# Kernel tuning notes

Hardware: AMD Instinct MI355X
Metric: run time of the kernel (lower is better)

The kernel has to match this reference:

```python
import jax, jax.numpy as jnp
import numpy as np

N_NODES = 100000
N_EDGES = 1600000
IN_CH = 128
HID = 128
OUT_CH = 2
NUM_GRAPHS = 512


def _mlp_params(key, d_in, d_out):
    k1, k2 = jax.random.split(key)
    s1 = 1.0 / np.sqrt(d_in)
    s2 = 1.0 / np.sqrt(d_out)
    return (jax.random.uniform(k1, (d_in, d_out), jnp.float32, -s1, s1),
            jnp.zeros((d_out,), jnp.float32),
            jax.random.uniform(k2, (d_out, d_out), jnp.float32, -s2, s2),
            jnp.zeros((d_out,), jnp.float32))


def setup_inputs() -> dict:
    key = jax.random.key(0)
    ks = jax.random.split(key, 8)
    x = jax.random.normal(ks[0], (N_NODES, IN_CH), jnp.float32)
    edge_index = jax.random.randint(ks[1], (2, N_EDGES), 0, N_NODES, jnp.int64)
    batch = jnp.sort(jax.random.randint(ks[2], (N_NODES,), 0, NUM_GRAPHS, jnp.int64))
    w1_0, b1_0, w2_0, b2_0 = _mlp_params(ks[3], IN_CH, HID)
    w1_1, b1_1, w2_1, b2_1 = _mlp_params(ks[4], HID, HID)
    w1_2, b1_2, w2_2, b2_2 = _mlp_params(ks[5], HID, HID)
    s = 1.0 / np.sqrt(HID)
    w_lin = jax.random.uniform(ks[6], (HID, OUT_CH), jnp.float32, -s, s)
    b_lin = jnp.zeros((OUT_CH,), jnp.float32)
    return {"x": x, "edge_index": edge_index, "batch": batch,
            "w1_0": w1_0, "b1_0": b1_0, "w2_0": w2_0, "b2_0": b2_0,
            "w1_1": w1_1, "b1_1": b1_1, "w2_1": w2_1, "b2_1": b2_1,
            "w1_2": w1_2, "b1_2": b1_2, "w2_2": w2_2, "b2_2": b2_2,
            "w_lin": w_lin, "b_lin": b_lin}


def _gin_conv(x, src, dst, w1, b1, w2, b2):
    # GINConv with eps=0: MLP(x + sum_{j in N(i)} x_j)
    agg = jax.ops.segment_sum(x[src], dst, num_segments=N_NODES)  # [N, d]
    h = x + agg
    h = jax.nn.relu(h @ w1 + b1)
    return h @ w2 + b2


def reference(x, edge_index, batch,
              w1_0, b1_0, w2_0, b2_0,
              w1_1, b1_1, w2_1, b2_1,
              w1_2, b1_2, w2_2, b2_2,
              w_lin, b_lin):
    src, dst = edge_index[0], edge_index[1]
    h = _gin_conv(x, src, dst, w1_0, b1_0, w2_0, b2_0)
    h = jax.nn.relu(h)
    h = jax.nn.relu(_gin_conv(h, src, dst, w1_1, b1_1, w2_1, b2_1))
    h = jax.nn.relu(h)  # forward applies relu twice after GIN1
    h = _gin_conv(h, src, dst, w1_2, b1_2, w2_2, b2_2)
    # global mean pool per graph
    sums = jax.ops.segment_sum(h, batch, num_segments=NUM_GRAPHS)  # [G, d]
    counts = jax.ops.segment_sum(jnp.ones((N_NODES,), h.dtype), batch,
                                 num_segments=NUM_GRAPHS)
    pooled = sums / jnp.maximum(counts, 1.0)[:, None]
    # dropout is identity in eval mode
    return pooled @ w_lin + b_lin  # [G, OUT_CH]
```

## Files before the change

### kernel.cpp

```cpp
#include <hip/hip_runtime.h>
#include <hip/hip_bf16.h>

#define N_NODES   100000
#define N_EDGES   1600000
#define IN_CH     128
#define HID       128
#define OUT_CH    2
#define NUM_GRAPHS 512

#define BKT_SHIFT 9
#define NB2 ((N_NODES + 511) >> BKT_SHIFT)
#define PB  200
#define CHUNK (N_EDGES / PB)

#define NCAST (N_NODES * IN_CH / 4 / 256)

typedef __attribute__((ext_vector_type(8))) short bf16x8;
typedef __attribute__((ext_vector_type(4))) float f32x4;
typedef unsigned int uint32;
typedef unsigned long long uint64;

static __device__ __forceinline__ float b2f(uint32 b) {
    return __uint_as_float(b << 16);
}
static __device__ __forceinline__ unsigned short f2b(float f) {
    uint32 u = __float_as_uint(f);
    u += 0x7fffu + ((u >> 16) & 1u);
    return (unsigned short)(u >> 16);
}
static __device__ __forceinline__ void acc8(float* a, int4 v) {
    uint32 x;
    x = (uint32)v.x; a[0] += __uint_as_float(x << 16); a[1] += __uint_as_float(x & 0xffff0000u);
    x = (uint32)v.y; a[2] += __uint_as_float(x << 16); a[3] += __uint_as_float(x & 0xffff0000u);
    x = (uint32)v.z; a[4] += __uint_as_float(x << 16); a[5] += __uint_as_float(x & 0xffff0000u);
    x = (uint32)v.w; a[6] += __uint_as_float(x << 16); a[7] += __uint_as_float(x & 0xffff0000u);
}

__global__ void k_front(const float* __restrict__ x, unsigned short* __restrict__ h,
                        const float* w0, const float* w1, const float* w2,
                        const float* w3, const float* w4, const float* w5,
                        unsigned short* __restrict__ wt,
                        const int* __restrict__ dst, int* __restrict__ histG) {
    __shared__ int hist[NB2];
    int bid = blockIdx.x, t = threadIdx.x;
    if (bid < NCAST) {
        int base = (bid * 256 + t) * 4;
        float4 v = *(const float4*)(x + base);
        ushort4 o;
        o.x = f2b(v.x); o.y = f2b(v.y); o.z = f2b(v.z); o.w = f2b(v.w);
        *(ushort4*)(h + base) = o;
    } else if (bid < NCAST + 6) {
        const float* ws[6] = {w0, w1, w2, w3, w4, w5};
        int wi = bid - NCAST;
        const float* w = ws[wi];
        unsigned short* o = wt + wi * 16384;
        for (int i = t; i < 16384; i += 256) {
            int k = i >> 7, n = i & 127;
            o[n * 128 + k] = f2b(w[i]);
        }
    } else {
        int blk = bid - NCAST - 6;
        for (int i = t; i < NB2; i += 256) hist[i] = 0;
        __syncthreads();
        int base = blk * CHUNK;
        for (int i = t; i < CHUNK; i += 256)
            atomicAdd(&hist[dst[base + i] >> BKT_SHIFT], 1);
        __syncthreads();
        for (int i = t; i < NB2; i += 256) histG[i * PB + blk] = hist[i];
    }
}

__global__ void k_scan1(const int* __restrict__ in, int* __restrict__ out,
                        int* __restrict__ bsum, int n) {
    __shared__ int sm[256];
    int b = blockIdx.x, t = threadIdx.x;
    int base = b * 1024 + t * 4;
    int v0 = 0, v1 = 0, v2 = 0, v3 = 0;
    if (base + 3 < n) {
        int4 q = *(const int4*)(in + base);
        v0 = q.x; v1 = q.y; v2 = q.z; v3 = q.w;
    } else {
        if (base + 0 < n) v0 = in[base + 0];
        if (base + 1 < n) v1 = in[base + 1];
        if (base + 2 < n) v2 = in[base + 2];
        if (base + 3 < n) v3 = in[base + 3];
    }
    int s = v0 + v1 + v2 + v3;
    sm[t] = s;
    __syncthreads();
    for (int off = 1; off < 256; off <<= 1) {
        int u = (t >= off) ? sm[t - off] : 0;
        __syncthreads();
        sm[t] += u;
        __syncthreads();
    }
    int p = (t == 0) ? 0 : sm[t - 1];
    int o0 = p, o1 = p + v0, o2 = o1 + v1, o3 = o2 + v2;
    if (base + 3 < n) {
        *(int4*)(out + base) = make_int4(o0, o1, o2, o3);
    } else {
        if (base + 0 < n) out[base + 0] = o0;
        if (base + 1 < n) out[base + 1] = o1;
        if (base + 2 < n) out[base + 2] = o2;
        if (base + 3 < n) out[base + 3] = o3;
    }
    if (t == 255) bsum[b] = s + ((t == 0) ? 0 : sm[t - 1]);
}

__global__ void k_scan3b(int* __restrict__ out, const int* __restrict__ bsum, int n) {
    __shared__ int add_s;
    int b = blockIdx.x, t = threadIdx.x;
    if (t == 0) {
        int s = 0;
        for (int i = 0; i < b; ++i) s += bsum[i];
        add_s = s;
    }
    __syncthreads();
    int add = add_s;
    int base = b * 1024 + t * 4;
    if (base + 3 < n) {
        int4 q = *(const int4*)(out + base);
        q.x += add; q.y += add; q.z += add; q.w += add;
        *(int4*)(out + base) = q;
    } else {
        for (int j = 0; j < 4; ++j)
            if (base + j < n) out[base + j] += add;
    }
}

__global__ void k_p3g(const int* __restrict__ ei, const int* __restrict__ baseG,
                      uint64* __restrict__ ebuf,
                      const int* __restrict__ batch, int* __restrict__ goff) {
    __shared__ int cur[NB2];
    int t = threadIdx.x, blk = blockIdx.x;
    if (blk >= PB) {
        int g = (blk - PB) * 512 + t;
        if (g <= NUM_GRAPHS) {
            int lo = 0, hi = N_NODES;
            while (lo < hi) {
                int mid = (lo + hi) >> 1;
                if (batch[mid] < g) lo = mid + 1; else hi = mid;
            }
            goff[g] = lo;
        }
        return;
    }
    for (int i = t; i < NB2; i += 512) cur[i] = baseG[i * PB + blk];
    __syncthreads();
    int base = blk * CHUNK;
    for (int i = t; i < CHUNK; i += 512) {
        int e = base + i;
        int src = ei[e];
        int dst = ei[N_EDGES + e];
        int pos = atomicAdd(&cur[dst >> BKT_SHIFT], 1);
        ebuf[pos] = ((uint64)(uint32)dst << 32) | (uint32)src;
    }
}

__global__ void k_p4(const uint64* __restrict__ ebuf, const int* __restrict__ baseG,
                     int* __restrict__ off, int* __restrict__ csr) {
    __shared__ int ldeg[512];
    __shared__ int lscan[512];
    __shared__ int lcur[512];
    int b = blockIdx.x, t = threadIdx.x;
    int node0 = b << BKT_SHIFT;
    int nn = min(512, N_NODES - node0);
    int e0 = baseG[b * PB];
    int e1 = (b == NB2 - 1) ? N_EDGES : baseG[(b + 1) * PB];
    ldeg[t] = 0;
    __syncthreads();
    for (int e = e0 + t; e < e1; e += 512) {
        int dst = (int)(ebuf[e] >> 32);
        atomicAdd(&ldeg[dst - node0], 1);
    }
    __syncthreads();
    lscan[t] = ldeg[t];
    __syncthreads();
    for (int o = 1; o < 512; o <<= 1) {
        int v = (t >= o) ? lscan[t - o] : 0;
        __syncthreads();
        lscan[t] += v;
        __syncthreads();
    }
    int excl = (t == 0) ? 0 : lscan[t - 1];
    lcur[t] = e0 + excl;
    if (t < nn) off[node0 + t] = e0 + excl;
    if (b == NB2 - 1 && t == 0) off[N_NODES] = N_EDGES;
    __syncthreads();
    for (int e = e0 + t; e < e1; e += 512) {
        uint64 pr = ebuf[e];
        int dst = (int)(pr >> 32);
        int pos = atomicAdd(&lcur[dst - node0], 1);
        csr[pos] = (int)(pr & 0xffffffffu);
    }
}

__global__ void k_agg(const unsigned short* __restrict__ h,
                      const int* __restrict__ off, const int* __restrict__ csr,
                      unsigned short* __restrict__ hs) {
    int wid = (blockIdx.x * 256 + threadIdx.x) >> 6;
    int lane = threadIdx.x & 63;
    if (wid >= N_NODES) return;
    int g = lane >> 4, sub = lane & 15;
    int e0 = off[wid], e1 = off[wid + 1];
    float a[8] = {0.f, 0.f, 0.f, 0.f, 0.f, 0.f, 0.f, 0.f};
    int e = e0 + g;
    if (e + 12 < e1) {
        int s0 = csr[e], s1 = csr[e + 4], s2 = csr[e + 8], s3 = csr[e + 12];
        e += 16;
        while (e + 12 < e1) {
            int t0 = csr[e], t1 = csr[e + 4], t2 = csr[e + 8], t3 = csr[e + 12];
            int4 v0 = *(const int4*)(h + (size_t)s0 * 128 + sub * 8);
            int4 v1 = *(const int4*)(h + (size_t)s1 * 128 + sub * 8);
            int4 v2 = *(const int4*)(h + (size_t)s2 * 128 + sub * 8);
            int4 v3 = *(const int4*)(h + (size_t)s3 * 128 + sub * 8);
            acc8(a, v0); acc8(a, v1); acc8(a, v2); acc8(a, v3);
            s0 = t0; s1 = t1; s2 = t2; s3 = t3;
            e += 16;
        }
        int4 v0 = *(const int4*)(h + (size_t)s0 * 128 + sub * 8);
        int4 v1 = *(const int4*)(h + (size_t)s1 * 128 + sub * 8);
        int4 v2 = *(const int4*)(h + (size_t)s2 * 128 + sub * 8);
        int4 v3 = *(const int4*)(h + (size_t)s3 * 128 + sub * 8);
        acc8(a, v0); acc8(a, v1); acc8(a, v2); acc8(a, v3);
    }
    for (; e + 4 < e1; e += 8) {
        int s0 = csr[e];
        int s1 = csr[e + 4];
        int4 v0 = *(const int4*)(h + (size_t)s0 * 128 + sub * 8);
        int4 v1 = *(const int4*)(h + (size_t)s1 * 128 + sub * 8);
        acc8(a, v0);
        acc8(a, v1);
    }
    if (e < e1) {
        int s0 = csr[e];
        int4 v0 = *(const int4*)(h + (size_t)s0 * 128 + sub * 8);
        acc8(a, v0);
    }
#pragma unroll
    for (int j = 0; j < 8; ++j) {
        a[j] += __shfl_xor(a[j], 16);
        a[j] += __shfl_xor(a[j], 32);
    }
    if (g == 0) {
        int4 sv = *(const int4*)(h + (size_t)wid * 128 + sub * 8);
        acc8(a, sv);
        int4 o;
        o.x = (int)((uint32)f2b(a[0]) | ((uint32)f2b(a[1]) << 16));
        o.y = (int)((uint32)f2b(a[2]) | ((uint32)f2b(a[3]) << 16));
        o.z = (int)((uint32)f2b(a[4]) | ((uint32)f2b(a[5]) << 16));
        o.w = (int)((uint32)f2b(a[6]) | ((uint32)f2b(a[7]) << 16));
        *(int4*)(hs + (size_t)wid * 128 + sub * 8) = o;
    }
}

template<int OUTER_RELU>
__global__ void k_mlp(const unsigned short* __restrict__ hs,
                      const unsigned short* __restrict__ w1t, const float* __restrict__ b1,
                      const unsigned short* __restrict__ w2t, const float* __restrict__ b2,
                      unsigned short* __restrict__ ho) {
    __shared__ unsigned short T[64 * 128];
    int tid = threadIdx.x;
    int lane = tid & 63, wave = tid >> 6;
    int l15 = lane & 15, l4 = lane >> 4;
    int row0 = blockIdx.x * 64;
    int wn0 = wave * 32;

    bf16x8 w1f[2][4], w2f[2][4];
#pragma unroll
    for (int nt = 0; nt < 2; ++nt)
#pragma unroll
        for (int k = 0; k < 4; ++k) {
            int o = (wn0 + nt * 16 + l15) * 128 + k * 32 + l4 * 8;
            w1f[nt][k] = *(const bf16x8*)(w1t + o);
            w2f[nt][k] = *(const bf16x8*)(w2t + o);
        }
    float bias1[2] = { b1[wn0 + l15], b1[wn0 + 16 + l15] };
    float bias2[2] = { b2[wn0 + l15], b2[wn0 + 16 + l15] };

#pragma unroll
    for (int mt = 0; mt < 4; ++mt) {
        int arow = row0 + mt * 16 + l15;
        if (arow >= N_NODES) arow = N_NODES - 1;
        const unsigned short* ap = hs + (size_t)arow * 128 + l4 * 8;
        bf16x8 a0 = *(const bf16x8*)(ap);
        bf16x8 a1 = *(const bf16x8*)(ap + 32);
        bf16x8 a2 = *(const bf16x8*)(ap + 64);
        bf16x8 a3 = *(const bf16x8*)(ap + 96);
#pragma unroll
        for (int nt = 0; nt < 2; ++nt) {
            f32x4 acc = {0.f, 0.f, 0.f, 0.f};
            acc = __builtin_amdgcn_mfma_f32_16x16x32_bf16(a0, w1f[nt][0], acc, 0, 0, 0);
            acc = __builtin_amdgcn_mfma_f32_16x16x32_bf16(a1, w1f[nt][1], acc, 0, 0, 0);
            acc = __builtin_amdgcn_mfma_f32_16x16x32_bf16(a2, w1f[nt][2], acc, 0, 0, 0);
            acc = __builtin_amdgcn_mfma_f32_16x16x32_bf16(a3, w1f[nt][3], acc, 0, 0, 0);
#pragma unroll
            for (int j = 0; j < 4; ++j) {
                float v = fmaxf(acc[j] + bias1[nt], 0.f);
                int trow = mt * 16 + l4 * 4 + j;
                int tcol = wn0 + nt * 16 + l15;
                int byte = (trow * 256 + tcol * 2) ^ ((trow & 7) << 4);
                *(unsigned short*)((char*)T + byte) = f2b(v);
            }
        }
    }
    __syncthreads();

#pragma unroll
    for (int mt = 0; mt < 4; ++mt) {
        int trow = mt * 16 + l15;
        int sw = (trow & 7) << 4;
        int rb = trow * 256 + l4 * 16;
        bf16x8 t0 = *(const bf16x8*)((const char*)T + ((rb + 0)   ^ sw));
        bf16x8 t1 = *(const bf16x8*)((const char*)T + ((rb + 64)  ^ sw));
        bf16x8 t2 = *(const bf16x8*)((const char*)T + ((rb + 128) ^ sw));
        bf16x8 t3 = *(const bf16x8*)((const char*)T + ((rb + 192) ^ sw));
        __syncthreads();
#pragma unroll
        for (int nt = 0; nt < 2; ++nt) {
            f32x4 acc = {0.f, 0.f, 0.f, 0.f};
            acc = __builtin_amdgcn_mfma_f32_16x16x32_bf16(t0, w2f[nt][0], acc, 0, 0, 0);
            acc = __builtin_amdgcn_mfma_f32_16x16x32_bf16(t1, w2f[nt][1], acc, 0, 0, 0);
            acc = __builtin_amdgcn_mfma_f32_16x16x32_bf16(t2, w2f[nt][2], acc, 0, 0, 0);
            acc = __builtin_amdgcn_mfma_f32_16x16x32_bf16(t3, w2f[nt][3], acc, 0, 0, 0);
#pragma unroll
            for (int j = 0; j < 4; ++j) {
                float v = acc[j] + bias2[nt];
                if (OUTER_RELU) v = fmaxf(v, 0.f);
                int orow = mt * 16 + l4 * 4 + j;
                int ocol = wn0 + nt * 16 + l15;
                int byte = (orow * 256 + ocol * 2) ^ ((orow & 7) << 4);
                *(unsigned short*)((char*)T + byte) = f2b(v);
            }
        }
    }
    __syncthreads();

    for (int c = tid; c < 1024; c += 256) {
        int r = c >> 4, cc = c & 15;
        int byte = (r * 256 + cc * 16) ^ ((r & 7) << 4);
        int4 v = *(const int4*)((const char*)T + byte);
        int gr = row0 + r;
        if (gr < N_NODES)
            *(int4*)(ho + (size_t)gr * 128 + cc * 8) = v;
    }
}

__global__ void k_pool(const unsigned short* __restrict__ h,
                       const int* __restrict__ goff,
                       const float* __restrict__ wl, const float* __restrict__ bl,
                       float* __restrict__ out) {
    int g = blockIdx.x;
    int lane = threadIdx.x;
    int e0 = goff[g], e1 = goff[g + 1];
    int c2 = lane << 1;
    float s0 = 0.f, s1 = 0.f;
    int r = e0;
    for (; r + 3 < e1; r += 4) {
        uint32 v0 = *(const uint32*)(h + (size_t)r * 128 + c2);
        uint32 v1 = *(const uint32*)(h + (size_t)(r + 1) * 128 + c2);
        uint32 v2 = *(const uint32*)(h + (size_t)(r + 2) * 128 + c2);
        uint32 v3 = *(const uint32*)(h + (size_t)(r + 3) * 128 + c2);
        s0 += b2f(v0 & 0xffffu) + b2f(v1 & 0xffffu) + b2f(v2 & 0xffffu) + b2f(v3 & 0xffffu);
        s1 += b2f(v0 >> 16) + b2f(v1 >> 16) + b2f(v2 >> 16) + b2f(v3 >> 16);
    }
    for (; r < e1; ++r) {
        uint32 v = *(const uint32*)(h + (size_t)r * 128 + c2);
        s0 += b2f(v & 0xffffu);
        s1 += b2f(v >> 16);
    }
    float inv = 1.f / fmaxf((float)(e1 - e0), 1.f);
    s0 *= inv; s1 *= inv;
    float o0 = s0 * wl[c2 * 2]     + s1 * wl[(c2 + 1) * 2];
    float o1 = s0 * wl[c2 * 2 + 1] + s1 * wl[(c2 + 1) * 2 + 1];
#pragma unroll
    for (int d = 32; d; d >>= 1) {
        o0 += __shfl_down(o0, d);
        o1 += __shfl_down(o1, d);
    }
    if (lane == 0) {
        out[g * 2]     = o0 + bl[0];
        out[g * 2 + 1] = o1 + bl[1];
    }
}

extern "C" void kernel_launch(void* const* d_in, const int* in_sizes, int n_in,
                              void* d_out, int out_size, void* d_ws, size_t ws_size,
                              hipStream_t stream) {
    const float* x     = (const float*)d_in[0];
    const int*   ei    = (const int*)d_in[1];
    const int*   batch = (const int*)d_in[2];
    const float* w1[3] = {(const float*)d_in[3],  (const float*)d_in[7],  (const float*)d_in[11]};
    const float* b1[3] = {(const float*)d_in[4],  (const float*)d_in[8],  (const float*)d_in[12]};
    const float* w2[3] = {(const float*)d_in[5],  (const float*)d_in[9],  (const float*)d_in[13]};
    const float* b2[3] = {(const float*)d_in[6],  (const float*)d_in[10], (const float*)d_in[14]};
    const float* wl    = (const float*)d_in[15];
    const float* bl    = (const float*)d_in[16];

    char* p = (char*)d_ws;
    auto alloc = [&](size_t bytes) {
        char* r = p;
        p += (bytes + 255) & ~(size_t)255;
        return r;
    };
    int* off    = (int*)alloc((size_t)(N_NODES + 1) * 4);
    int* goff   = (int*)alloc((size_t)(NUM_GRAPHS + 1) * 4);
    int* histG  = (int*)alloc((size_t)(NB2 * PB) * 4);
    int* baseG  = (int*)alloc((size_t)(NB2 * PB + 1) * 4);
    int* bsum   = (int*)alloc((size_t)128 * 4);
    int* csr    = (int*)alloc((size_t)N_EDGES * 4);
    unsigned short* wts = (unsigned short*)alloc((size_t)6 * 16384 * 2);
    unsigned short* hA  = (unsigned short*)alloc((size_t)N_NODES * 128 * 2);
    unsigned short* hS  = (unsigned short*)alloc((size_t)N_NODES * 128 * 2);
    unsigned short* hB  = (unsigned short*)alloc((size_t)N_NODES * 128 * 2);
    uint64* ebuf = (uint64*)hS;

    k_front<<<NCAST + 6 + PB, 256, 0, stream>>>(x, hA,
        w1[0], w2[0], w1[1], w2[1], w1[2], w2[2], wts, ei + N_EDGES, histG);

    const int SCAN_N = NB2 * PB;
    const int SCAN_BLOCKS = (SCAN_N + 1023) / 1024;
    k_scan1<<<SCAN_BLOCKS, 256, 0, stream>>>(histG, baseG, bsum, SCAN_N);
    k_scan3b<<<SCAN_BLOCKS, 256, 0, stream>>>(baseG, bsum, SCAN_N);
    k_p3g<<<PB + 2, 512, 0, stream>>>(ei, baseG, ebuf, batch, goff);
    k_p4<<<NB2, 512, 0, stream>>>(ebuf, baseG, off, csr);

    unsigned short* wt1[3] = {wts,             wts + 2 * 16384, wts + 4 * 16384};
    unsigned short* wt2[3] = {wts + 1 * 16384, wts + 3 * 16384, wts + 5 * 16384};

    const int AGG_GRID = N_NODES / 4;
    const int MLP_GRID = (N_NODES + 63) / 64;

    k_agg<<<AGG_GRID, 256, 0, stream>>>(hA, off, csr, hS);
    k_mlp<1><<<MLP_GRID, 256, 0, stream>>>(hS, wt1[0], b1[0], wt2[0], b2[0], hB);
    k_agg<<<AGG_GRID, 256, 0, stream>>>(hB, off, csr, hS);
    k_mlp<1><<<MLP_GRID, 256, 0, stream>>>(hS, wt1[1], b1[1], wt2[1], b2[1], hA);
    k_agg<<<AGG_GRID, 256, 0, stream>>>(hA, off, csr, hS);
    k_mlp<0><<<MLP_GRID, 256, 0, stream>>>(hS, wt1[2], b1[2], wt2[2], b2[2], hB);

    k_pool<<<NUM_GRAPHS, 64, 0, stream>>>(hB, goff, wl, bl, (float*)d_out);
}
```

Before: 362.3 us.

## Remap aggregation kernel to process column slices of 4 nodes per wave

```diff
diff --git a/kernel.cpp b/kernel.cpp
--- a/kernel.cpp
+++ b/kernel.cpp
@@ -198,59 +198,58 @@
 __global__ void k_agg(const unsigned short* __restrict__ h,
                       const int* __restrict__ off, const int* __restrict__ csr,
                       unsigned short* __restrict__ hs) {
-    int wid = (blockIdx.x * 256 + threadIdx.x) >> 6;
+    int bid = blockIdx.x;
+    int s = bid & 3;
+    int nb = (bid >> 2) << 4;
+    int wave = threadIdx.x >> 6;
+    int n0 = nb + wave * 4;
     int lane = threadIdx.x & 63;
-    if (wid >= N_NODES) return;
-    int g = lane >> 4, sub = lane & 15;
-    int e0 = off[wid], e1 = off[wid + 1];
-    float a[8] = {0.f, 0.f, 0.f, 0.f, 0.f, 0.f, 0.f, 0.f};
-    int e = e0 + g;
-    if (e + 12 < e1) {
-        int s0 = csr[e], s1 = csr[e + 4], s2 = csr[e + 8], s3 = csr[e + 12];
-        e += 16;
-        while (e + 12 < e1) {
-            int t0 = csr[e], t1 = csr[e + 4], t2 = csr[e + 8], t3 = csr[e + 12];
-            int4 v0 = *(const int4*)(h + (size_t)s0 * 128 + sub * 8);
-            int4 v1 = *(const int4*)(h + (size_t)s1 * 128 + sub * 8);
-            int4 v2 = *(const int4*)(h + (size_t)s2 * 128 + sub * 8);
-            int4 v3 = *(const int4*)(h + (size_t)s3 * 128 + sub * 8);
-            acc8(a, v0); acc8(a, v1); acc8(a, v2); acc8(a, v3);
-            s0 = t0; s1 = t1; s2 = t2; s3 = t3;
-            e += 16;
-        }
-        int4 v0 = *(const int4*)(h + (size_t)s0 * 128 + sub * 8);
-        int4 v1 = *(const int4*)(h + (size_t)s1 * 128 + sub * 8);
-        int4 v2 = *(const int4*)(h + (size_t)s2 * 128 + sub * 8);
-        int4 v3 = *(const int4*)(h + (size_t)s3 * 128 + sub * 8);
-        acc8(a, v0); acc8(a, v1); acc8(a, v2); acc8(a, v3);
-    }
-    for (; e + 4 < e1; e += 8) {
-        int s0 = csr[e];
-        int s1 = csr[e + 4];
-        int4 v0 = *(const int4*)(h + (size_t)s0 * 128 + sub * 8);
-        int4 v1 = *(const int4*)(h + (size_t)s1 * 128 + sub * 8);
-        acc8(a, v0);
-        acc8(a, v1);
-    }
-    if (e < e1) {
-        int s0 = csr[e];
-        int4 v0 = *(const int4*)(h + (size_t)s0 * 128 + sub * 8);
-        acc8(a, v0);
-    }
-#pragma unroll
-    for (int j = 0; j < 8; ++j) {
-        a[j] += __shfl_xor(a[j], 16);
-        a[j] += __shfl_xor(a[j], 32);
-    }
-    if (g == 0) {
-        int4 sv = *(const int4*)(h + (size_t)wid * 128 + sub * 8);
-        acc8(a, sv);
-        int4 o;
-        o.x = (int)((uint32)f2b(a[0]) | ((uint32)f2b(a[1]) << 16));
-        o.y = (int)((uint32)f2b(a[2]) | ((uint32)f2b(a[3]) << 16));
-        o.z = (int)((uint32)f2b(a[4]) | ((uint32)f2b(a[5]) << 16));
-        o.w = (int)((uint32)f2b(a[6]) | ((uint32)f2b(a[7]) << 16));
-        *(int4*)(hs + (size_t)wid * 128 + sub * 8) = o;
+    int g = lane >> 2, sub = lane & 3;
+    int co = s * 64 + sub * 16;
+
+    int o0 = off[n0], o1 = off[n0 + 1], o2 = off[n0 + 2], o3 = off[n0 + 3], o4 = off[n0 + 4];
+
+    float A0[8] = {0,0,0,0,0,0,0,0}, A1[8] = {0,0,0,0,0,0,0,0};
+    float A2[8] = {0,0,0,0,0,0,0,0}, A3[8] = {0,0,0,0,0,0,0,0};
+    int e0 = o0 + g, e1 = o1 + g, e2 = o2 + g, e3 = o3 + g;
+
+    while (__any((e0 < o1) | (e1 < o2) | (e2 < o3) | (e3 < o4))) {
+        int4 v0, v1, v2, v3;
+        bool a0 = e0 < o1, a1 = e1 < o2, a2 = e2 < o3, a3 = e3 < o4;
+        if (a0) { int src = csr[e0]; v0 = *(const int4*)((const char*)h + (size_t)src * 256 + co); }
+        if (a1) { int src = csr[e1]; v1 = *(const int4*)((const char*)h + (size_t)src * 256 + co); }
+        if (a2) { int src = csr[e2]; v2 = *(const int4*)((const char*)h + (size_t)src * 256 + co); }
+        if (a3) { int src = csr[e3]; v3 = *(const int4*)((const char*)h + (size_t)src * 256 + co); }
+        if (a0) { acc8(A0, v0); e0 += 16; }
+        if (a1) { acc8(A1, v1); e1 += 16; }
+        if (a2) { acc8(A2, v2); e2 += 16; }
+        if (a3) { acc8(A3, v3); e3 += 16; }
+    }
+#pragma unroll
+    for (int k = 0; k < 8; ++k) {
+        A0[k] += __shfl_xor(A0[k], 4);  A0[k] += __shfl_xor(A0[k], 8);
+        A0[k] += __shfl_xor(A0[k], 16); A0[k] += __shfl_xor(A0[k], 32);
+        A1[k] += __shfl_xor(A1[k], 4);  A1[k] += __shfl_xor(A1[k], 8);
+        A1[k] += __shfl_xor(A1[k], 16); A1[k] += __shfl_xor(A1[k], 32);
+        A2[k] += __shfl_xor(A2[k], 4);  A2[k] += __shfl_xor(A2[k], 8);
+        A2[k] += __shfl_xor(A2[k], 16); A2[k] += __shfl_xor(A2[k], 32);
+        A3[k] += __shfl_xor(A3[k], 4);  A3[k] += __shfl_xor(A3[k], 8);
+        A3[k] += __shfl_xor(A3[k], 16); A3[k] += __shfl_xor(A3[k], 32);
+    }
+#pragma unroll
+    for (int j = 0; j < 4; ++j) {
+        if (g == j) {
+            float* A = (j == 0) ? A0 : (j == 1) ? A1 : (j == 2) ? A2 : A3;
+            int node = n0 + j;
+            int4 sv = *(const int4*)((const char*)h + (size_t)node * 256 + co);
+            acc8(A, sv);
+            int4 o;
+            o.x = (int)((uint32)f2b(A[0]) | ((uint32)f2b(A[1]) << 16));
+            o.y = (int)((uint32)f2b(A[2]) | ((uint32)f2b(A[3]) << 16));
+            o.z = (int)((uint32)f2b(A[4]) | ((uint32)f2b(A[5]) << 16));
+            o.w = (int)((uint32)f2b(A[6]) | ((uint32)f2b(A[7]) << 16));
+            *(int4*)((char*)hs + (size_t)node * 256 + co) = o;
+        }
     }
 }
 
@@ -428,7 +427,7 @@
     unsigned short* wt1[3] = {wts,             wts + 2 * 16384, wts + 4 * 16384};
     unsigned short* wt2[3] = {wts + 1 * 16384, wts + 3 * 16384, wts + 5 * 16384};
 
-    const int AGG_GRID = N_NODES / 4;
+    const int AGG_GRID = (N_NODES / 16) * 4;
     const int MLP_GRID = (N_NODES + 63) / 64;
 
     k_agg<<<AGG_GRID, 256, 0, stream>>>(hA, off, csr, hS);
```

After: 637.8 us. +76.1%, slower.
